# Performance work log

Measured on AMD Instinct MI355X. Metric: run time of the kernel, lower is better.

## Reference

```python
import jax, jax.numpy as jnp
import numpy as np

N_NODES = 100000
N_EDGES = 1600000
IN_F, HID, OUT_F = 256, 128, 48
ALPHA = 0.01
K = 10
# SparseDropout with dropout_prob=0 keeps all edges but scales by 1/(1-0+1e-5)
DROP_SCALE = 1.0 / (1.0 + 1e-5)


def setup_inputs() -> dict:
    key = jax.random.key(0)
    ks = jax.random.split(key, 8)
    x = jax.random.normal(ks[0], (N_NODES, IN_F), dtype=jnp.float32)
    rows = jax.random.randint(ks[1], (N_EDGES,), 0, N_NODES, dtype=jnp.int32)
    cols = jax.random.randint(ks[2], (N_EDGES,), 0, N_NODES, dtype=jnp.int32)
    vals = jax.random.uniform(ks[3], (N_EDGES,), dtype=jnp.float32)
    # Linear params (Kaiming-uniform-ish like torch defaults)
    lim1 = 1.0 / np.sqrt(IN_F)
    W1 = jax.random.uniform(ks[4], (IN_F, HID), minval=-lim1, maxval=lim1, dtype=jnp.float32)
    b1 = jax.random.uniform(ks[5], (HID,), minval=-lim1, maxval=lim1, dtype=jnp.float32)
    lim2 = 1.0 / np.sqrt(HID)
    W2 = jax.random.uniform(ks[6], (HID, OUT_F), minval=-lim2, maxval=lim2, dtype=jnp.float32)
    b2 = jax.random.uniform(ks[7], (OUT_F,), minval=-lim2, maxval=lim2, dtype=jnp.float32)
    return {"x": x, "rows": rows, "cols": cols, "vals": vals,
            "W1": W1, "b1": b1, "W2": W2, "b2": b2}


def reference(x, rows, cols, vals, W1, b1, W2, b2):
    # MLP (dropout=0 -> identity)
    h = jax.nn.relu(x @ W1 + b1)          # [N, HID]
    h = h @ W2 + b2                        # [N, OUT_F]
    v = vals * DROP_SCALE                  # SparseDropout(p=0) value scaling
    # K-step APPNP propagation: h <- (1-alpha) * A @ h + alpha * h
    def step(h, _):
        ah = jax.ops.segment_sum(v[:, None] * h[cols], rows, num_segments=N_NODES)
        return (1.0 - ALPHA) * ah + ALPHA * h, None
    h, _ = jax.lax.scan(step, h, None, length=K)
    return h
```

## Files before the change

### kernel.cpp

```cpp
#include <hip/hip_runtime.h>

#define N_NODES 100000
#define N_EDGES 1600000
#define IN_F 256
#define HID 128
#define OUT_F 48
#define PAD_F 64
#define ALPHA 0.01f
#define K_STEPS 10
#define DROP_SCALE (1.0f / (1.0f + 1e-5f))

#define NBUCK 196
#define BCAP 10240
#define EPB 4096
#define ROW_MASK_CLR 0xFFFFFFFFFC01FFFFULL

typedef __bf16 v8bf __attribute__((ext_vector_type(8)));
typedef float v4f __attribute__((ext_vector_type(4)));
typedef unsigned long long u64;

static __device__ __forceinline__ __bf16 tobf(float f) { return (__bf16)f; }

__global__ __launch_bounds__(256) void conv_w(const float* __restrict__ W1,
                                              const float* __restrict__ W2,
                                              __bf16* __restrict__ w1t,
                                              __bf16* __restrict__ w2t) {
  int i = blockIdx.x * 256 + threadIdx.x;
  if (i < HID * IN_F) {
    int n = i >> 8, k = i & 255;
    w1t[i] = tobf(W1[k * HID + n]);
  }
  int j = i - HID * IN_F;
  if (j >= 0 && j < OUT_F * HID) {
    int n = j >> 7, k = j & 127;
    w2t[j] = tobf(W2[k * OUT_F + n]);
  }
}

__global__ __launch_bounds__(256) void mlp_mfma(
    const float* __restrict__ x, const __bf16* __restrict__ w1t,
    const float* __restrict__ b1, const __bf16* __restrict__ w2t,
    const float* __restrict__ b2, __bf16* __restrict__ h0) {
  __shared__ __bf16 h1s[64][136];

  const int tid = threadIdx.x;
  const int wv = tid >> 6;
  const int l = tid & 63;
  const int lm = l & 15;
  const int ko = (l >> 4) * 8;
  const int gw = blockIdx.x * 4 + wv;
  if (gw >= N_NODES / 16) return;
  const int n0w = gw * 16;
  const int xrow = n0w + lm;

  v4f acc1[8];
#pragma unroll
  for (int nf = 0; nf < 8; nf++) acc1[nf] = (v4f){0.f, 0.f, 0.f, 0.f};

  const float* xb = x + (size_t)xrow * IN_F + ko;
#pragma unroll
  for (int kh = 0; kh < 2; kh++) {
    float4 xr[8];
#pragma unroll
    for (int k0 = 0; k0 < 4; k0++) {
      const float* p = xb + (kh * 4 + k0) * 32;
      xr[2 * k0] = *(const float4*)p;
      xr[2 * k0 + 1] = *(const float4*)(p + 4);
    }
#pragma unroll
    for (int k0 = 0; k0 < 4; k0++) {
      const float* f0 = (const float*)&xr[2 * k0];
      v8bf a;
#pragma unroll
      for (int j = 0; j < 8; j++) a[j] = tobf(f0[j]);
      const __bf16* w1base = w1t + (size_t)lm * IN_F + (kh * 4 + k0) * 32 + ko;
#pragma unroll
      for (int nf = 0; nf < 8; nf++) {
        v8bf b = *(const v8bf*)(w1base + nf * 16 * IN_F);
        acc1[nf] = __builtin_amdgcn_mfma_f32_16x16x32_bf16(a, b, acc1[nf], 0, 0, 0);
      }
    }
  }

#pragma unroll
  for (int nf = 0; nf < 8; nf++) {
    float bb = b1[nf * 16 + lm];
#pragma unroll
    for (int q = 0; q < 4; q++) {
      int rr = (wv << 4) + (l >> 4) * 4 + q;
      h1s[rr][nf * 16 + lm] = tobf(fmaxf(acc1[nf][q] + bb, 0.f));
    }
  }
  __syncthreads();

  const int lrow = (wv << 4) + lm;
  v4f acc2[3];
#pragma unroll
  for (int nf = 0; nf < 3; nf++) acc2[nf] = (v4f){0.f, 0.f, 0.f, 0.f};
  const __bf16* w2base = w2t + (size_t)lm * HID + ko;
#pragma unroll
  for (int k0 = 0; k0 < 4; k0++) {
    v8bf a = *(const v8bf*)&h1s[lrow][k0 * 32 + ko];
#pragma unroll
    for (int nf = 0; nf < 3; nf++) {
      v8bf b = *(const v8bf*)(w2base + nf * 16 * HID + k0 * 32);
      acc2[nf] = __builtin_amdgcn_mfma_f32_16x16x32_bf16(a, b, acc2[nf], 0, 0, 0);
    }
  }
#pragma unroll
  for (int nf = 0; nf < 3; nf++) {
    float bb = b2[nf * 16 + lm];
#pragma unroll
    for (int q = 0; q < 4; q++) {
      int node = n0w + (l >> 4) * 4 + q;
      h0[(size_t)node * PAD_F + nf * 16 + lm] = tobf(acc2[nf][q] + bb);
    }
  }
  if (l < 32) {
    uint4 z = make_uint4(0, 0, 0, 0);
    *(uint4*)(h0 + (size_t)(n0w + (l >> 1)) * PAD_F + 48 + (l & 1) * 8) = z;
  }
}

__global__ __launch_bounds__(256) void bucket_kernel(
    const int* __restrict__ rows, const int* __restrict__ cols,
    const float* __restrict__ vals, int* __restrict__ bcur,
    u64* __restrict__ brec) {
  __shared__ int lhist[NBUCK];
  __shared__ int lbase[NBUCK];
  const int t = threadIdx.x;
  const int base = blockIdx.x * EPB;

  for (int i = t; i < NBUCK; i += 256) lhist[i] = 0;
  __syncthreads();

  u64 rec[16];
  short bb[16];
  short pp[16];
#pragma unroll
  for (int j = 0; j < 4; j++) {
    int e = base + j * 1024 + t * 4;
    bool ok = e < N_EDGES;
    int4 r4 = ok ? *(const int4*)(rows + e) : make_int4(0, 0, 0, 0);
    int4 c4 = ok ? *(const int4*)(cols + e) : make_int4(0, 0, 0, 0);
    float4 v4 = ok ? *(const float4*)(vals + e) : make_float4(0, 0, 0, 0);
    int rr[4] = {r4.x, r4.y, r4.z, r4.w};
    int cc[4] = {c4.x, c4.y, c4.z, c4.w};
    float vv[4] = {v4.x, v4.y, v4.z, v4.w};
#pragma unroll
    for (int q = 0; q < 4; q++) {
      int idx = j * 4 + q;
      int b = rr[q] >> 9;
      float v = vv[q] * (DROP_SCALE * (1.0f - ALPHA));
      rec[idx] = ((u64)__float_as_uint(v) << 32) |
                 ((u64)(rr[q] & 511) << 17) | (unsigned)cc[q];
      bb[idx] = ok ? (short)b : (short)-1;
      pp[idx] = ok ? (short)atomicAdd(&lhist[b], 1) : (short)0;
    }
  }
  __syncthreads();

  for (int i = t; i < NBUCK; i += 256) {
    int n = lhist[i];
    lbase[i] = (n > 0) ? atomicAdd(&bcur[i * 16], n) : 0;
  }
  __syncthreads();

#pragma unroll
  for (int j = 0; j < 16; j++) {
    if (bb[j] >= 0)
      brec[(size_t)bb[j] * BCAP + lbase[bb[j]] + pp[j]] = rec[j];
  }
}

__global__ __launch_bounds__(256) void bscan_kernel(const int* __restrict__ bcur,
                                                    int* __restrict__ bstart,
                                                    int* __restrict__ rowptr) {
  __shared__ int s[256];
  int t = threadIdx.x;
  int v = (t < NBUCK) ? bcur[t * 16] : 0;
  s[t] = v;
  __syncthreads();
  for (int off = 1; off < 256; off <<= 1) {
    int add = (t >= off) ? s[t - off] : 0;
    __syncthreads();
    s[t] += add;
    __syncthreads();
  }
  if (t < NBUCK) bstart[t] = s[t] - v;
  if (t == 0) rowptr[N_NODES] = N_EDGES;
}

__global__ __launch_bounds__(512) void csr_kernel(
    const int* __restrict__ bcur, const int* __restrict__ bstart,
    const u64* __restrict__ brec, int* __restrict__ rowptr,
    u64* __restrict__ edges) {
  __shared__ int cnt[512];
  __shared__ int sc[512];
  const int b = blockIdx.x;
  const int t = threadIdx.x;
  const int n = bcur[b * 16];
  const int base = bstart[b];
  const size_t boff = (size_t)b * BCAP;

  cnt[t] = 0;
  __syncthreads();
  for (int i = t; i < n; i += 512)
    atomicAdd(&cnt[(int)((brec[boff + i] >> 17) & 511)], 1);
  __syncthreads();

  int v = cnt[t];
  sc[t] = v;
  __syncthreads();
  for (int off = 1; off < 512; off <<= 1) {
    int add = (t >= off) ? sc[t - off] : 0;
    __syncthreads();
    sc[t] += add;
    __syncthreads();
  }
  int excl = sc[t] - v;
  int grow = b * 512 + t;
  if (grow < N_NODES) rowptr[grow] = base + excl;
  cnt[t] = excl;
  __syncthreads();

  for (int i = t; i < n; i += 512) {
    u64 rec = brec[boff + i];
    int rr = (int)((rec >> 17) & 511);
    int p = atomicAdd(&cnt[rr], 1);
    edges[base + p] = rec & ROW_MASK_CLR;
  }
}

template <int FINAL>
__global__ __launch_bounds__(256) void prop_kernel(
    const __bf16* __restrict__ hin, __bf16* __restrict__ hout,
    float* __restrict__ fout, const int* __restrict__ rowptr,
    const u64* __restrict__ edges) {
  int wid = (blockIdx.x * 256 + threadIdx.x) >> 6;
  int lane = threadIdx.x & 63;
  if (wid >= N_NODES) return;
  const int g = lane >> 3;
  const int t = lane & 7;
  int s = __builtin_amdgcn_readfirstlane(rowptr[wid]);
  int e = __builtin_amdgcn_readfirstlane(rowptr[wid + 1]);

  float acc[8];
#pragma unroll
  for (int j = 0; j < 8; j++) acc[j] = 0.f;

  if (g == 0) {
    uint4 q = *(const uint4*)(hin + (size_t)wid * PAD_F + t * 8);
    unsigned uu[4] = {q.x, q.y, q.z, q.w};
#pragma unroll
    for (int k = 0; k < 4; k++) {
      acc[2 * k] = ALPHA * __uint_as_float(uu[k] << 16);
      acc[2 * k + 1] = ALPHA * __uint_as_float(uu[k] & 0xffff0000u);
    }
  }

  int i = s + g;
  for (; i + 8 < e; i += 16) {
    u64 r0 = edges[i];
    u64 r1 = edges[i + 8];
    int c0 = (int)(r0 & 0xffffffffu);
    int c1 = (int)(r1 & 0xffffffffu);
    float v0 = __uint_as_float((unsigned)(r0 >> 32));
    float v1 = __uint_as_float((unsigned)(r1 >> 32));
    uint4 q0 = *(const uint4*)(hin + (size_t)c0 * PAD_F + t * 8);
    uint4 q1 = *(const uint4*)(hin + (size_t)c1 * PAD_F + t * 8);
    unsigned a0[4] = {q0.x, q0.y, q0.z, q0.w};
    unsigned a1[4] = {q1.x, q1.y, q1.z, q1.w};
#pragma unroll
    for (int k = 0; k < 4; k++) {
      acc[2 * k] = fmaf(v0, __uint_as_float(a0[k] << 16), acc[2 * k]);
      acc[2 * k + 1] = fmaf(v0, __uint_as_float(a0[k] & 0xffff0000u), acc[2 * k + 1]);
    }
#pragma unroll
    for (int k = 0; k < 4; k++) {
      acc[2 * k] = fmaf(v1, __uint_as_float(a1[k] << 16), acc[2 * k]);
      acc[2 * k + 1] = fmaf(v1, __uint_as_float(a1[k] & 0xffff0000u), acc[2 * k + 1]);
    }
  }
  if (i < e) {
    u64 r0 = edges[i];
    int c0 = (int)(r0 & 0xffffffffu);
    float v0 = __uint_as_float((unsigned)(r0 >> 32));
    uint4 q0 = *(const uint4*)(hin + (size_t)c0 * PAD_F + t * 8);
    unsigned a0[4] = {q0.x, q0.y, q0.z, q0.w};
#pragma unroll
    for (int k = 0; k < 4; k++) {
      acc[2 * k] = fmaf(v0, __uint_as_float(a0[k] << 16), acc[2 * k]);
      acc[2 * k + 1] = fmaf(v0, __uint_as_float(a0[k] & 0xffff0000u), acc[2 * k + 1]);
    }
  }

#pragma unroll
  for (int m = 8; m <= 32; m <<= 1) {
#pragma unroll
    for (int j = 0; j < 8; j++) acc[j] += __shfl_xor(acc[j], m, 64);
  }

  if (g == 0) {
    if (FINAL) {
      if (t < 6) {
        float* dst = fout + (size_t)wid * OUT_F + t * 8;
        v4f lo4 = {acc[0], acc[1], acc[2], acc[3]};
        v4f hi4 = {acc[4], acc[5], acc[6], acc[7]};
        __builtin_nontemporal_store(lo4, (v4f*)dst);
        __builtin_nontemporal_store(hi4, (v4f*)(dst + 4));
      }
    } else {
      unsigned w[4];
#pragma unroll
      for (int k = 0; k < 4; k++) {
        unsigned short lo = __builtin_bit_cast(unsigned short, (__bf16)acc[2 * k]);
        unsigned short hi = __builtin_bit_cast(unsigned short, (__bf16)acc[2 * k + 1]);
        w[k] = ((unsigned)hi << 16) | lo;
      }
      *(uint4*)(hout + (size_t)wid * PAD_F + t * 8) =
          make_uint4(w[0], w[1], w[2], w[3]);
    }
  }
}

extern "C" void kernel_launch(void* const* d_in, const int* in_sizes, int n_in,
                              void* d_out, int out_size, void* d_ws,
                              size_t ws_size, hipStream_t stream) {
  const float* x = (const float*)d_in[0];
  const int* rows = (const int*)d_in[1];
  const int* cols = (const int*)d_in[2];
  const float* vals = (const float*)d_in[3];
  const float* W1 = (const float*)d_in[4];
  const float* b1 = (const float*)d_in[5];
  const float* W2 = (const float*)d_in[6];
  const float* b2 = (const float*)d_in[7];
  float* out = (float*)d_out;

  char* ws = (char*)d_ws;
  const size_t HA_OFF = 0;
  const size_t HB_OFF = 12800000;
  const size_t EDGES_OFF = 25600000;
  const size_t BREC_OFF = 38400000;
  const size_t ROWPTR_OFF = 54456320;
  const size_t BCUR_OFF = 54856448;
  const size_t BSTART_OFF = 54868992;
  const size_t W1T_OFF = 54870016;
  const size_t W2T_OFF = 54935552;

  __bf16* hA = (__bf16*)(ws + HA_OFF);
  __bf16* hB = (__bf16*)(ws + HB_OFF);
  u64* edges = (u64*)(ws + EDGES_OFF);
  u64* brec = (u64*)(ws + BREC_OFF);
  int* rowptr = (int*)(ws + ROWPTR_OFF);
  int* bcur = (int*)(ws + BCUR_OFF);
  int* bstart = (int*)(ws + BSTART_OFF);
  __bf16* w1t = (__bf16*)(ws + W1T_OFF);
  __bf16* w2t = (__bf16*)(ws + W2T_OFF);

  conv_w<<<(HID * IN_F + OUT_F * HID + 255) / 256, 256, 0, stream>>>(W1, W2,
                                                                     w1t, w2t);
  mlp_mfma<<<(N_NODES / 16 + 3) / 4, 256, 0, stream>>>(x, w1t, b1, w2t, b2, hA);

  (void)hipMemsetAsync(bcur, 0, NBUCK * 64, stream);
  bucket_kernel<<<(N_EDGES + EPB - 1) / EPB, 256, 0, stream>>>(rows, cols, vals,
                                                               bcur, brec);
  bscan_kernel<<<1, 256, 0, stream>>>(bcur, bstart, rowptr);
  csr_kernel<<<NBUCK, 512, 0, stream>>>(bcur, bstart, brec, rowptr, edges);

  const int PROP_BLOCKS = (N_NODES * 64 + 255) / 256;
  for (int k = 0; k < K_STEPS - 1; k++) {
    const __bf16* hin = (k & 1) ? hB : hA;
    __bf16* hout = (k & 1) ? hA : hB;
    prop_kernel<0><<<PROP_BLOCKS, 256, 0, stream>>>(hin, hout, nullptr, rowptr,
                                                    edges);
  }
  prop_kernel<1><<<PROP_BLOCKS, 256, 0, stream>>>(hB, nullptr, out, rowptr,
                                                  edges);
}
```

Baseline: 540.0 us.

## Fuse MLP and edge bucketing into one horizontally-partitioned kernel launch

Merges the MLP MFMA kernel and the edge bucketing kernel into a single launch, with blocks split by blockIdx between the two independent jobs so they run concurrently. This removes one launch and the serialization gap between two independent stages. The MLP path now loads all 256 x features up front (16 float4 registers) instead of in two halves, and a launch_bounds occupancy hint of 4 is added. The cost is higher register pressure and shared memory shared by both roles, which may lower occupancy for the bucket blocks.

```diff
diff --git a/kernel.cpp b/kernel.cpp
--- a/kernel.cpp
+++ b/kernel.cpp
@@ -15,6 +15,9 @@
 #define EPB 4096
 #define ROW_MASK_CLR 0xFFFFFFFFFC01FFFFULL
 
+#define MLP_BLOCKS ((N_NODES / 16 + 3) / 4)
+#define BUCKET_BLOCKS ((N_EDGES + EPB - 1) / EPB)
+
 typedef __bf16 v8bf __attribute__((ext_vector_type(8)));
 typedef float v4f __attribute__((ext_vector_type(4)));
 typedef unsigned long long u64;
@@ -37,139 +40,137 @@
   }
 }
 
-__global__ __launch_bounds__(256) void mlp_mfma(
+__global__ __launch_bounds__(256, 4) void fused_mlp_bucket(
     const float* __restrict__ x, const __bf16* __restrict__ w1t,
     const float* __restrict__ b1, const __bf16* __restrict__ w2t,
-    const float* __restrict__ b2, __bf16* __restrict__ h0) {
+    const float* __restrict__ b2, __bf16* __restrict__ h0,
+    const int* __restrict__ rows, const int* __restrict__ cols,
+    const float* __restrict__ vals, int* __restrict__ bcur,
+    u64* __restrict__ brec) {
   __shared__ __bf16 h1s[64][136];
+  __shared__ int lhist[NBUCK];
+  __shared__ int lbase[NBUCK];
 
   const int tid = threadIdx.x;
-  const int wv = tid >> 6;
-  const int l = tid & 63;
-  const int lm = l & 15;
-  const int ko = (l >> 4) * 8;
-  const int gw = blockIdx.x * 4 + wv;
-  if (gw >= N_NODES / 16) return;
-  const int n0w = gw * 16;
-  const int xrow = n0w + lm;
-
-  v4f acc1[8];
-#pragma unroll
-  for (int nf = 0; nf < 8; nf++) acc1[nf] = (v4f){0.f, 0.f, 0.f, 0.f};
-
-  const float* xb = x + (size_t)xrow * IN_F + ko;
-#pragma unroll
-  for (int kh = 0; kh < 2; kh++) {
-    float4 xr[8];
-#pragma unroll
-    for (int k0 = 0; k0 < 4; k0++) {
-      const float* p = xb + (kh * 4 + k0) * 32;
-      xr[2 * k0] = *(const float4*)p;
-      xr[2 * k0 + 1] = *(const float4*)(p + 4);
-    }
-#pragma unroll
-    for (int k0 = 0; k0 < 4; k0++) {
+
+  if (blockIdx.x < MLP_BLOCKS) {
+    const int wv = tid >> 6;
+    const int l = tid & 63;
+    const int lm = l & 15;
+    const int ko = (l >> 4) * 8;
+    const int gw = blockIdx.x * 4 + wv;
+    if (gw >= N_NODES / 16) return;
+    const int n0w = gw * 16;
+    const int xrow = n0w + lm;
+
+    const float* xb = x + (size_t)xrow * IN_F + ko;
+    float4 xr[16];
+#pragma unroll
+    for (int k0 = 0; k0 < 8; k0++) {
+      xr[2 * k0] = *(const float4*)(xb + k0 * 32);
+      xr[2 * k0 + 1] = *(const float4*)(xb + k0 * 32 + 4);
+    }
+
+    v4f acc1[8];
+#pragma unroll
+    for (int nf = 0; nf < 8; nf++) acc1[nf] = (v4f){0.f, 0.f, 0.f, 0.f};
+
+#pragma unroll
+    for (int k0 = 0; k0 < 8; k0++) {
       const float* f0 = (const float*)&xr[2 * k0];
       v8bf a;
 #pragma unroll
       for (int j = 0; j < 8; j++) a[j] = tobf(f0[j]);
-      const __bf16* w1base = w1t + (size_t)lm * IN_F + (kh * 4 + k0) * 32 + ko;
+      const __bf16* w1base = w1t + (size_t)lm * IN_F + k0 * 32 + ko;
 #pragma unroll
       for (int nf = 0; nf < 8; nf++) {
         v8bf b = *(const v8bf*)(w1base + nf * 16 * IN_F);
         acc1[nf] = __builtin_amdgcn_mfma_f32_16x16x32_bf16(a, b, acc1[nf], 0, 0, 0);
       }
     }
-  }
-
-#pragma unroll
-  for (int nf = 0; nf < 8; nf++) {
-    float bb = b1[nf * 16 + lm];
-#pragma unroll
-    for (int q = 0; q < 4; q++) {
-      int rr = (wv << 4) + (l >> 4) * 4 + q;
-      h1s[rr][nf * 16 + lm] = tobf(fmaxf(acc1[nf][q] + bb, 0.f));
-    }
-  }
-  __syncthreads();
-
-  const int lrow = (wv << 4) + lm;
-  v4f acc2[3];
-#pragma unroll
-  for (int nf = 0; nf < 3; nf++) acc2[nf] = (v4f){0.f, 0.f, 0.f, 0.f};
-  const __bf16* w2base = w2t + (size_t)lm * HID + ko;
-#pragma unroll
-  for (int k0 = 0; k0 < 4; k0++) {
-    v8bf a = *(const v8bf*)&h1s[lrow][k0 * 32 + ko];
+
+#pragma unroll
+    for (int nf = 0; nf < 8; nf++) {
+      float bb = b1[nf * 16 + lm];
+#pragma unroll
+      for (int q = 0; q < 4; q++) {
+        int rr = (wv << 4) + (l >> 4) * 4 + q;
+        h1s[rr][nf * 16 + lm] = tobf(fmaxf(acc1[nf][q] + bb, 0.f));
+      }
+    }
+    __syncthreads();
+
+    const int lrow = (wv << 4) + lm;
+    v4f acc2[3];
+#pragma unroll
+    for (int nf = 0; nf < 3; nf++) acc2[nf] = (v4f){0.f, 0.f, 0.f, 0.f};
+    const __bf16* w2base = w2t + (size_t)lm * HID + ko;
+#pragma unroll
+    for (int k0 = 0; k0 < 4; k0++) {
+      v8bf a = *(const v8bf*)&h1s[lrow][k0 * 32 + ko];
+#pragma unroll
+      for (int nf = 0; nf < 3; nf++) {
+        v8bf b = *(const v8bf*)(w2base + nf * 16 * HID + k0 * 32);
+        acc2[nf] = __builtin_amdgcn_mfma_f32_16x16x32_bf16(a, b, acc2[nf], 0, 0, 0);
+      }
+    }
 #pragma unroll
     for (int nf = 0; nf < 3; nf++) {
-      v8bf b = *(const v8bf*)(w2base + nf * 16 * HID + k0 * 32);
-      acc2[nf] = __builtin_amdgcn_mfma_f32_16x16x32_bf16(a, b, acc2[nf], 0, 0, 0);
-    }
-  }
-#pragma unroll
-  for (int nf = 0; nf < 3; nf++) {
-    float bb = b2[nf * 16 + lm];
-#pragma unroll
-    for (int q = 0; q < 4; q++) {
-      int node = n0w + (l >> 4) * 4 + q;
-      h0[(size_t)node * PAD_F + nf * 16 + lm] = tobf(acc2[nf][q] + bb);
-    }
-  }
-  if (l < 32) {
-    uint4 z = make_uint4(0, 0, 0, 0);
-    *(uint4*)(h0 + (size_t)(n0w + (l >> 1)) * PAD_F + 48 + (l & 1) * 8) = z;
-  }
-}
-
-__global__ __launch_bounds__(256) void bucket_kernel(
-    const int* __restrict__ rows, const int* __restrict__ cols,
-    const float* __restrict__ vals, int* __restrict__ bcur,
-    u64* __restrict__ brec) {
-  __shared__ int lhist[NBUCK];
-  __shared__ int lbase[NBUCK];
-  const int t = threadIdx.x;
-  const int base = blockIdx.x * EPB;
-
-  for (int i = t; i < NBUCK; i += 256) lhist[i] = 0;
-  __syncthreads();
-
-  u64 rec[16];
-  short bb[16];
-  short pp[16];
-#pragma unroll
-  for (int j = 0; j < 4; j++) {
-    int e = base + j * 1024 + t * 4;
-    bool ok = e < N_EDGES;
-    int4 r4 = ok ? *(const int4*)(rows + e) : make_int4(0, 0, 0, 0);
-    int4 c4 = ok ? *(const int4*)(cols + e) : make_int4(0, 0, 0, 0);
-    float4 v4 = ok ? *(const float4*)(vals + e) : make_float4(0, 0, 0, 0);
-    int rr[4] = {r4.x, r4.y, r4.z, r4.w};
-    int cc[4] = {c4.x, c4.y, c4.z, c4.w};
-    float vv[4] = {v4.x, v4.y, v4.z, v4.w};
-#pragma unroll
-    for (int q = 0; q < 4; q++) {
-      int idx = j * 4 + q;
-      int b = rr[q] >> 9;
-      float v = vv[q] * (DROP_SCALE * (1.0f - ALPHA));
-      rec[idx] = ((u64)__float_as_uint(v) << 32) |
-                 ((u64)(rr[q] & 511) << 17) | (unsigned)cc[q];
-      bb[idx] = ok ? (short)b : (short)-1;
-      pp[idx] = ok ? (short)atomicAdd(&lhist[b], 1) : (short)0;
-    }
-  }
-  __syncthreads();
-
-  for (int i = t; i < NBUCK; i += 256) {
-    int n = lhist[i];
-    lbase[i] = (n > 0) ? atomicAdd(&bcur[i * 16], n) : 0;
-  }
-  __syncthreads();
-
-#pragma unroll
-  for (int j = 0; j < 16; j++) {
-    if (bb[j] >= 0)
-      brec[(size_t)bb[j] * BCAP + lbase[bb[j]] + pp[j]] = rec[j];
+      float bb = b2[nf * 16 + lm];
+#pragma unroll
+      for (int q = 0; q < 4; q++) {
+        int node = n0w + (l >> 4) * 4 + q;
+        h0[(size_t)node * PAD_F + nf * 16 + lm] = tobf(acc2[nf][q] + bb);
+      }
+    }
+    if (l < 32) {
+      uint4 z = make_uint4(0, 0, 0, 0);
+      *(uint4*)(h0 + (size_t)(n0w + (l >> 1)) * PAD_F + 48 + (l & 1) * 8) = z;
+    }
+  } else {
+    const int bid = blockIdx.x - MLP_BLOCKS;
+    const int base = bid * EPB;
+
+    for (int i = tid; i < NBUCK; i += 256) lhist[i] = 0;
+    __syncthreads();
+
+    u64 rec[16];
+    short bb[16];
+    short pp[16];
+#pragma unroll
+    for (int j = 0; j < 4; j++) {
+      int e = base + j * 1024 + tid * 4;
+      bool ok = e < N_EDGES;
+      int4 r4 = ok ? *(const int4*)(rows + e) : make_int4(0, 0, 0, 0);
+      int4 c4 = ok ? *(const int4*)(cols + e) : make_int4(0, 0, 0, 0);
+      float4 v4 = ok ? *(const float4*)(vals + e) : make_float4(0, 0, 0, 0);
+      int rr[4] = {r4.x, r4.y, r4.z, r4.w};
+      int cc[4] = {c4.x, c4.y, c4.z, c4.w};
+      float vv[4] = {v4.x, v4.y, v4.z, v4.w};
+#pragma unroll
+      for (int q = 0; q < 4; q++) {
+        int idx = j * 4 + q;
+        int b = rr[q] >> 9;
+        float v = vv[q] * (DROP_SCALE * (1.0f - ALPHA));
+        rec[idx] = ((u64)__float_as_uint(v) << 32) |
+                   ((u64)(rr[q] & 511) << 17) | (unsigned)cc[q];
+        bb[idx] = ok ? (short)b : (short)-1;
+        pp[idx] = ok ? (short)atomicAdd(&lhist[b], 1) : (short)0;
+      }
+    }
+    __syncthreads();
+
+    for (int i = tid; i < NBUCK; i += 256) {
+      int n = lhist[i];
+      lbase[i] = (n > 0) ? atomicAdd(&bcur[i * 16], n) : 0;
+    }
+    __syncthreads();
+
+#pragma unroll
+    for (int j = 0; j < 16; j++) {
+      if (bb[j] >= 0)
+        brec[(size_t)bb[j] * BCAP + lbase[bb[j]] + pp[j]] = rec[j];
+    }
   }
 }
 
@@ -360,11 +361,11 @@
 
   conv_w<<<(HID * IN_F + OUT_F * HID + 255) / 256, 256, 0, stream>>>(W1, W2,
                                                                      w1t, w2t);
-  mlp_mfma<<<(N_NODES / 16 + 3) / 4, 256, 0, stream>>>(x, w1t, b1, w2t, b2, hA);
-
   (void)hipMemsetAsync(bcur, 0, NBUCK * 64, stream);
-  bucket_kernel<<<(N_EDGES + EPB - 1) / EPB, 256, 0, stream>>>(rows, cols, vals,
-                                                               bcur, brec);
+
+  fused_mlp_bucket<<<MLP_BLOCKS + BUCKET_BLOCKS, 256, 0, stream>>>(
+      x, w1t, b1, w2t, b2, hA, rows, cols, vals, bcur, brec);
+
   bscan_kernel<<<1, 256, 0, stream>>>(bcur, bstart, rowptr);
   csr_kernel<<<NBUCK, 512, 0, stream>>>(bcur, bstart, brec, rowptr, edges);
 
```

Result: faster. 526.2 us (-2.6%).
